# Performance work log

Measured on AMD Instinct MI355X. Metric: run time of the kernel, lower is better.

The kernel has to match this reference:

```python
import jax, jax.numpy as jnp
import numpy as np

B, N, DIM = 4, 8192, 1024
HEADS, DIM_HEAD = 16, 64


def setup_inputs() -> dict:
    key = jax.random.key(0)
    ks = jax.random.split(key, 6)
    s = 1.0 / np.sqrt(DIM_HEAD)
    so = 1.0 / np.sqrt(HEADS * DIM_HEAD)
    return {
        "x": jax.random.normal(ks[0], (B, N, DIM), dtype=jnp.float32),
        "Wq": jax.random.uniform(ks[1], (DIM_HEAD, DIM_HEAD), jnp.float32, -s, s),
        "Wk": jax.random.uniform(ks[2], (DIM_HEAD, DIM_HEAD), jnp.float32, -s, s),
        "Wv": jax.random.uniform(ks[3], (DIM_HEAD, DIM_HEAD), jnp.float32, -s, s),
        "Wo": jax.random.uniform(ks[4], (DIM, HEADS * DIM_HEAD), jnp.float32, -so, so),
        "bo": jax.random.uniform(ks[5], (DIM,), jnp.float32, -so, so),
    }


def reference(x, Wq, Wk, Wv, Wo, bo):
    Bs, Ns, Cs = x.shape
    # [B, H, N, Dh]
    xh = x.reshape(Bs, Ns, HEADS, DIM_HEAD).transpose(0, 2, 1, 3)
    # torch Linear: y = x @ W.T
    q = jnp.einsum('bhnd,ed->bhne', xh, Wq)
    k = jnp.einsum('bhnd,ed->bhne', xh, Wk)
    v = jnp.einsum('bhnd,ed->bhne', xh, Wv)
    # k^T v: [B, H, Dh, Dh], normalized by N (dropout is identity, p=0)
    dots = jnp.einsum('bhnd,bhne->bhde', k, v) / float(Ns)
    res = jnp.einsum('bhnd,bhde->bhne', q, dots)
    # b h n d -> b n (h d)
    res = res.transpose(0, 2, 1, 3).reshape(Bs, Ns, HEADS * DIM_HEAD)
    return res @ Wo.T + bo
```

## Files before the change

### kernel.cpp

```cpp
#include <hip/hip_runtime.h>

#define DIMC 1024
#define NSEQ 8192
#define DH 64

typedef __attribute__((ext_vector_type(8))) short short8;
typedef __attribute__((ext_vector_type(4))) float f32x4;

__device__ __forceinline__ short f2bf(float f) {
  union { float f; unsigned u; } v; v.f = f;
  unsigned r = v.u + 0x7FFFu + ((v.u >> 16) & 1u);
  return (short)(r >> 16);
}

__device__ __forceinline__ unsigned pack_bf2(float a, float b) {
  union { float f; unsigned u; } va, vb;
  va.f = a; vb.f = b;
  unsigned ua = va.u + 0x8000u;
  unsigned ub = vb.u + 0x8000u;
  return (ua >> 16) | (ub & 0xFFFF0000u);
}

__device__ __forceinline__ void gload_lds16(const void* g, void* l) {
  __builtin_amdgcn_global_load_lds(
      (const __attribute__((address_space(1))) void*)g,
      (__attribute__((address_space(3))) void*)l, 16, 0, 0);
}

__global__ __launch_bounds__(64) void gram_kernel(const float* __restrict__ x,
                                                  float* __restrict__ Gpart,
                                                  short* __restrict__ xbf) {
  int chunk = blockIdx.x, bh = blockIdx.y;
  int b = bh >> 4, h = bh & 15;
  int t = threadIdx.x;
  __shared__ __align__(16) float rows[16 * 64];
  const float* xb = x + ((size_t)b * NSEQ) * DIMC + h * DH;
  short* xo = xbf ? xbf + ((size_t)b * NSEQ) * DIMC + h * DH : (short*)0;
  int d0 = (t >> 3) * 8, e0 = (t & 7) * 8;
  float acc[8][8] = {};
  float4 v[4];
#pragma unroll
  for (int i = 0; i < 4; i++) {
    int f4 = i * 64 + t;
    v[i] = *(const float4*)(xb + (size_t)(chunk * 256 + (f4 >> 4)) * DIMC + (f4 & 15) * 4);
  }
  for (int it = 0; it < 16; it++) {
    __syncthreads();
#pragma unroll
    for (int i = 0; i < 4; i++) ((float4*)rows)[i * 64 + t] = v[i];
    __syncthreads();
    if (xo) {
#pragma unroll
      for (int i = 0; i < 4; i++) {
        int f4 = i * 64 + t;
        int row = chunk * 256 + it * 16 + (f4 >> 4), col = (f4 & 15) * 4;
        uint2 pw = {pack_bf2(v[i].x, v[i].y), pack_bf2(v[i].z, v[i].w)};
        *(uint2*)(xo + (size_t)row * DIMC + col) = pw;
      }
    }
    if (it < 15) {
      int nbase = chunk * 256 + (it + 1) * 16;
#pragma unroll
      for (int i = 0; i < 4; i++) {
        int f4 = i * 64 + t;
        v[i] = *(const float4*)(xb + (size_t)(nbase + (f4 >> 4)) * DIMC + (f4 & 15) * 4);
      }
    }
#pragma unroll
    for (int r = 0; r < 16; r++) {
      float xd[8], xe[8];
      *(float4*)&xd[0] = *(const float4*)&rows[r * 64 + d0];
      *(float4*)&xd[4] = *(const float4*)&rows[r * 64 + d0 + 4];
      *(float4*)&xe[0] = *(const float4*)&rows[r * 64 + e0];
      *(float4*)&xe[4] = *(const float4*)&rows[r * 64 + e0 + 4];
#pragma unroll
      for (int i = 0; i < 8; i++)
#pragma unroll
        for (int j = 0; j < 8; j++) acc[i][j] = fmaf(xd[i], xe[j], acc[i][j]);
    }
  }
  float* gp = Gpart + (size_t)chunk * (64 * 4096) + (size_t)bh * 4096;
#pragma unroll
  for (int i = 0; i < 8; i++)
#pragma unroll
    for (int j = 0; j < 8; j++) gp[(d0 + i) * 64 + e0 + j] = acc[i][j];
}

__global__ void reduce_g(const float* __restrict__ Gpart, float* __restrict__ G) {
  int i = blockIdx.x * 256 + threadIdx.x;
  float s = 0.f;
#pragma unroll
  for (int p = 0; p < 32; p++) s += Gpart[(size_t)p * (64 * 4096) + i];
  G[i] = s;
}

__global__ __launch_bounds__(256) void combine_kernel(
    const float* __restrict__ G, const float* __restrict__ Wq,
    const float* __restrict__ Wk, const float* __restrict__ Wv,
    const float* __restrict__ Wo, short* __restrict__ WbigT) {
  int bh = blockIdx.x, qt = blockIdx.y;
  int b = bh >> 4, h = bh & 15;
  int t = threadIdx.x;
  __shared__ __align__(16) float sG[4096];
  __shared__ __align__(16) float sW[4096];
  __shared__ __align__(16) float sA[4096];
  __shared__ __align__(16) float sM[4096];

  for (int i = t; i < 4096; i += 256) sG[i] = G[(size_t)bh * 4096 + i];
  for (int i = t; i < 4096; i += 256) sW[i] = Wk[i];
  __syncthreads();

  int d0 = (t >> 4) * 4, e0 = (t & 15) * 4;
  {
    float a[4][4] = {};
    for (int fg = 0; fg < 16; fg++) {
      float wk[4][4], g4[4][4];
#pragma unroll
      for (int i = 0; i < 4; i++) *(float4*)wk[i] = *(const float4*)&sW[(d0 + i) * 64 + fg * 4];
#pragma unroll
      for (int ff = 0; ff < 4; ff++) *(float4*)g4[ff] = *(const float4*)&sG[(fg * 4 + ff) * 64 + e0];
#pragma unroll
      for (int i = 0; i < 4; i++)
#pragma unroll
        for (int ff = 0; ff < 4; ff++)
#pragma unroll
          for (int j = 0; j < 4; j++) a[i][j] = fmaf(wk[i][ff], g4[ff][j], a[i][j]);
    }
#pragma unroll
    for (int i = 0; i < 4; i++)
#pragma unroll
      for (int j = 0; j < 4; j++) sA[(d0 + i) * 64 + e0 + j] = a[i][j];
  }
  __syncthreads();
  for (int i = t; i < 4096; i += 256) sW[i] = Wv[i];
  __syncthreads();
  {
    float a[4][4] = {};
    for (int fgi = 0; fgi < 16; fgi++) {
      int fg = (fgi + (t & 15)) & 15;
      float t1[4][4], wv[4][4];
#pragma unroll
      for (int i = 0; i < 4; i++) *(float4*)t1[i] = *(const float4*)&sA[(d0 + i) * 64 + fg * 4];
#pragma unroll
      for (int j = 0; j < 4; j++) *(float4*)wv[j] = *(const float4*)&sW[(e0 + j) * 64 + fg * 4];
#pragma unroll
      for (int i = 0; i < 4; i++)
#pragma unroll
        for (int j = 0; j < 4; j++)
#pragma unroll
          for (int ff = 0; ff < 4; ff++) a[i][j] = fmaf(t1[i][ff], wv[j][ff], a[i][j]);
    }
    __syncthreads();
#pragma unroll
    for (int i = 0; i < 4; i++)
#pragma unroll
      for (int j = 0; j < 4; j++) sG[(d0 + i) * 64 + e0 + j] = a[i][j];
  }
  __syncthreads();
  for (int i = t; i < 4096; i += 256) sW[i] = Wq[i];
  __syncthreads();
  {
    float a[4][4] = {};
    for (int f = 0; f < 64; f++) {
      float wq[4], t2[4];
      *(float4*)wq = *(const float4*)&sW[f * 64 + d0];
      *(float4*)t2 = *(const float4*)&sG[f * 64 + e0];
#pragma unroll
      for (int i = 0; i < 4; i++)
#pragma unroll
        for (int j = 0; j < 4; j++) a[i][j] = fmaf(wq[i], t2[j], a[i][j]);
    }
#pragma unroll
    for (int i = 0; i < 4; i++)
#pragma unroll
      for (int j = 0; j < 4; j++) sM[(d0 + i) * 64 + e0 + j] = a[i][j] * (1.0f / 8192.0f);
  }
  __syncthreads();
  int dd0 = (t & 15) * 4, cl0 = (t >> 4) * 4;
  for (int cc = qt * 2; cc < qt * 2 + 2; cc++) {
    int c0 = cc * 64;
    for (int i = t; i < 4096; i += 256)
      sW[i] = Wo[(size_t)(c0 + (i >> 6)) * DIMC + h * DH + (i & 63)];
    __syncthreads();
    float a[4][4] = {};
    for (int egi = 0; egi < 16; egi++) {
      int eg = (egi + (t & 15)) & 15;
      float m4[4][4], wo4[4][4];
#pragma unroll
      for (int i = 0; i < 4; i++) *(float4*)m4[i] = *(const float4*)&sM[(dd0 + i) * 64 + eg * 4];
#pragma unroll
      for (int j = 0; j < 4; j++) *(float4*)wo4[j] = *(const float4*)&sW[(cl0 + j) * 64 + eg * 4];
#pragma unroll
      for (int i = 0; i < 4; i++)
#pragma unroll
        for (int j = 0; j < 4; j++)
#pragma unroll
          for (int ff = 0; ff < 4; ff++) a[i][j] = fmaf(m4[i][ff], wo4[j][ff], a[i][j]);
    }
#pragma unroll
    for (int j = 0; j < 4; j++) {
      uint2 pw = {pack_bf2(a[0][j], a[1][j]), pack_bf2(a[2][j], a[3][j])};
      *(uint2*)&WbigT[((size_t)b << 20) + (size_t)(c0 + cl0 + j) * DIMC + h * DH + dd0] = pw;
    }
    __syncthreads();
  }
}

__global__ __launch_bounds__(256, 3) void gemm_small(
    const float* __restrict__ x, const short* __restrict__ WbigT,
    const float* __restrict__ bo, float* __restrict__ out) {
  int bid = blockIdx.x;
  int xcd = bid & 7, r = bid >> 3;
  int g = r >> 5, q = r & 31;
  int m_blk = g * 32 + xcd * 4 + (q >> 3);
  int n_blk = q & 7;
  int b = m_blk >> 6;
  int row0 = m_blk * 128;
  int c0 = n_blk * 128;

  __shared__ __align__(16) short As[128 * 32];
  __shared__ __align__(16) short Bs[128 * 32];

  int t = threadIdx.x;
  int lane = t & 63, wave = t >> 6;
  int wm = wave >> 1, wn = wave & 1;
  int quad = lane >> 4, ln = lane & 15;

  f32x4 acc[4][4];
#pragma unroll
  for (int i = 0; i < 4; i++)
#pragma unroll
    for (int j = 0; j < 4; j++) acc[i][j] = (f32x4){0.f, 0.f, 0.f, 0.f};

  const short* Bbase = WbigT + ((size_t)b << 20);

  int e_base[2], crow_[2], lc_[2];
#pragma unroll
  for (int L = 0; L < 2; L++) {
    int e = (wave * 2 + L) * 512 + lane * 8;
    e_base[L] = e;
    int crow = e >> 5;
    crow_[L] = crow;
    lc_[L] = ((e >> 3) & 3) ^ ((crow >> 1) & 3);
  }

  for (int kt = 0; kt < 32; kt++) {
    int k0 = kt * 32;
    __syncthreads();
#pragma unroll
    for (int L = 0; L < 2; L++)
      gload_lds16(Bbase + (size_t)(c0 + crow_[L]) * DIMC + k0 + lc_[L] * 8, &Bs[e_base[L]]);
#pragma unroll
    for (int qq = 0; qq < 2; qq++) {
      int elem = qq * 2048 + wave * 512 + lane * 8;
      int m = elem >> 5, kk = elem & 31;
      const float* gp = x + (size_t)(row0 + m) * DIMC + k0 + kk;
      float4 v0 = *(const float4*)gp;
      float4 v1 = *(const float4*)(gp + 4);
      unsigned w0 = pack_bf2(v0.x, v0.y), w1 = pack_bf2(v0.z, v0.w);
      unsigned w2 = pack_bf2(v1.x, v1.y), w3 = pack_bf2(v1.z, v1.w);
      unsigned tmp[4] = {w0, w1, w2, w3};
      int pe = ((elem >> 3) & 3) ^ ((m >> 1) & 3);
      *(short8*)&As[m * 32 + pe * 8] = *(short8*)tmp;
    }
    __syncthreads();
    short8 afrag[4], bfrag[4];
#pragma unroll
    for (int i = 0; i < 4; i++) {
      int ar = wm * 64 + i * 16 + ln;
      afrag[i] = *(const short8*)&As[ar * 32 + (quad ^ ((ar >> 1) & 3)) * 8];
      int br = wn * 64 + i * 16 + ln;
      bfrag[i] = *(const short8*)&Bs[br * 32 + (quad ^ ((br >> 1) & 3)) * 8];
    }
#pragma unroll
    for (int i = 0; i < 4; i++)
#pragma unroll
      for (int j = 0; j < 4; j++)
        acc[i][j] = __builtin_amdgcn_mfma_f32_16x16x32_bf16(afrag[i], bfrag[j], acc[i][j], 0, 0, 0);
  }

  float bov[4];
#pragma unroll
  for (int j = 0; j < 4; j++) bov[j] = bo[c0 + wn * 64 + j * 16 + ln];
#pragma unroll
  for (int i = 0; i < 4; i++)
#pragma unroll
    for (int j = 0; j < 4; j++) {
      int col = c0 + wn * 64 + j * 16 + ln;
#pragma unroll
      for (int rr = 0; rr < 4; rr++) {
        int row = row0 + wm * 64 + i * 16 + quad * 4 + rr;
        out[(size_t)row * DIMC + col] = acc[i][j][rr] + bov[j];
      }
    }
}

__global__ __launch_bounds__(256, 3) void gemm_big(
    const short* __restrict__ xbf, const short* __restrict__ WbigT,
    const float* __restrict__ bo, float* __restrict__ out) {
  int bid = blockIdx.x;
  int xcd = bid & 7, r = bid >> 3;
  int g = r >> 5, q = r & 31;
  int m_blk = g * 32 + xcd * 4 + (q >> 3);
  int n_blk = q & 7;
  int b = m_blk >> 6;
  int row0 = m_blk * 128;
  int c0 = n_blk * 128;

  __shared__ __align__(16) short As[128 * 32];
  __shared__ __align__(16) short Bs[128 * 32];

  int t = threadIdx.x;
  int lane = t & 63, wave = t >> 6;
  int wm = wave >> 1, wn = wave & 1;
  int quad = lane >> 4, ln = lane & 15;

  f32x4 acc[4][4];
#pragma unroll
  for (int i = 0; i < 4; i++)
#pragma unroll
    for (int j = 0; j < 4; j++) acc[i][j] = (f32x4){0.f, 0.f, 0.f, 0.f};

  const short* Bbase = WbigT + ((size_t)b << 20);

  int e_base[2];
  const short* Asrc[2];
  const short* Bsrc[2];
#pragma unroll
  for (int L = 0; L < 2; L++) {
    int e = (wave * 2 + L) * 512 + lane * 8;
    e_base[L] = e;
    int row = e >> 5;
    int lc = ((e >> 3) & 3) ^ ((row >> 1) & 3);
    Asrc[L] = xbf + (size_t)(row0 + row) * DIMC + lc * 8;
    Bsrc[L] = Bbase + (size_t)(c0 + row) * DIMC + lc * 8;
  }

  for (int kt = 0; kt < 32; kt++) {
    int k0 = kt * 32;
    __syncthreads();
#pragma unroll
    for (int L = 0; L < 2; L++) gload_lds16(Asrc[L] + k0, &As[e_base[L]]);
#pragma unroll
    for (int L = 0; L < 2; L++) gload_lds16(Bsrc[L] + k0, &Bs[e_base[L]]);
    __syncthreads();
    short8 afrag[4], bfrag[4];
#pragma unroll
    for (int i = 0; i < 4; i++) {
      int ar = wm * 64 + i * 16 + ln;
      afrag[i] = *(const short8*)&As[ar * 32 + (quad ^ ((ar >> 1) & 3)) * 8];
      int br = wn * 64 + i * 16 + ln;
      bfrag[i] = *(const short8*)&Bs[br * 32 + (quad ^ ((br >> 1) & 3)) * 8];
    }
#pragma unroll
    for (int i = 0; i < 4; i++)
#pragma unroll
      for (int j = 0; j < 4; j++)
        acc[i][j] = __builtin_amdgcn_mfma_f32_16x16x32_bf16(afrag[i], bfrag[j], acc[i][j], 0, 0, 0);
  }

  float bov[4];
#pragma unroll
  for (int j = 0; j < 4; j++) bov[j] = bo[c0 + wn * 64 + j * 16 + ln];
#pragma unroll
  for (int i = 0; i < 4; i++)
#pragma unroll
    for (int j = 0; j < 4; j++) {
      int col = c0 + wn * 64 + j * 16 + ln;
#pragma unroll
      for (int rr = 0; rr < 4; rr++) {
        int row = row0 + wm * 64 + i * 16 + quad * 4 + rr;
        out[(size_t)row * DIMC + col] = acc[i][j][rr] + bov[j];
      }
    }
}

extern "C" void kernel_launch(void* const* d_in, const int* in_sizes, int n_in,
                              void* d_out, int out_size, void* d_ws, size_t ws_size,
                              hipStream_t stream) {
  const float* x  = (const float*)d_in[0];
  const float* Wq = (const float*)d_in[1];
  const float* Wk = (const float*)d_in[2];
  const float* Wv = (const float*)d_in[3];
  const float* Wo = (const float*)d_in[4];
  const float* bo = (const float*)d_in[5];
  float* out = (float*)d_out;
  (void)in_sizes; (void)n_in; (void)out_size;

  if (ws_size >= ((size_t)105 << 20)) {
    short* xbf   = (short*)d_ws;
    float* Gpart = (float*)((char*)d_ws + ((size_t)64 << 20));
    float* G     = (float*)((char*)d_ws + ((size_t)96 << 20));
    short* WbigT = (short*)((char*)d_ws + ((size_t)97 << 20));
    gram_kernel<<<dim3(32, 64), 64, 0, stream>>>(x, Gpart, xbf);
    reduce_g<<<1024, 256, 0, stream>>>(Gpart, G);
    combine_kernel<<<dim3(64, 8), 256, 0, stream>>>(G, Wq, Wk, Wv, Wo, WbigT);
    gemm_big<<<2048, 256, 0, stream>>>(xbf, WbigT, bo, out);
  } else {
    float* Gpart = (float*)d_ws;
    float* G     = (float*)((char*)d_ws + ((size_t)32 << 20));
    short* WbigT = (short*)((char*)d_ws + ((size_t)33 << 20));
    gram_kernel<<<dim3(32, 64), 64, 0, stream>>>(x, Gpart, (short*)0);
    reduce_g<<<1024, 256, 0, stream>>>(Gpart, G);
    combine_kernel<<<dim3(64, 8), 256, 0, stream>>>(G, Wq, Wk, Wv, Wo, WbigT);
    gemm_small<<<2048, 256, 0, stream>>>(x, WbigT, bo, out);
  }
}
```

Before: 381.2 us.

## Rewrite big GEMM with 256x256 tiles, 512 threads and double-buffered async LDS loads

The final bf16 GEMM moves from 128x128 tiles with K=32 single-buffered steps to 256x256 tiles with K=64 steps. Loads go through global_load_lds into double-buffered LDS, and vmcnt waits let the next stage's copies overlap the MFMA work. Each wave now computes 128x64, so more MFMAs run per LDS fragment load, and s_setprio raises priority around the MFMA bursts. The grid shrinks to 512 blocks with 128KB of LDS per block, which costs occupancy, and the tail wave across the CUs may be uneven.

```diff
diff --git a/kernel.cpp b/kernel.cpp
--- a/kernel.cpp
+++ b/kernel.cpp
@@ -295,82 +295,102 @@
     }
 }
 
-__global__ __launch_bounds__(256, 3) void gemm_big(
+__global__ __launch_bounds__(512, 2) void gemm_big2(
     const short* __restrict__ xbf, const short* __restrict__ WbigT,
     const float* __restrict__ bo, float* __restrict__ out) {
   int bid = blockIdx.x;
   int xcd = bid & 7, r = bid >> 3;
-  int g = r >> 5, q = r & 31;
-  int m_blk = g * 32 + xcd * 4 + (q >> 3);
-  int n_blk = q & 7;
-  int b = m_blk >> 6;
-  int row0 = m_blk * 128;
-  int c0 = n_blk * 128;
-
-  __shared__ __align__(16) short As[128 * 32];
-  __shared__ __align__(16) short Bs[128 * 32];
+  int m_blk = xcd * 16 + (r >> 2);
+  int n_blk = r & 3;
+  int b = m_blk >> 5;
+  size_t row0 = (size_t)m_blk * 256;
+  int c0 = n_blk * 256;
+
+  __shared__ __align__(16) short As[2][256 * 64];
+  __shared__ __align__(16) short Bs[2][256 * 64];
 
   int t = threadIdx.x;
   int lane = t & 63, wave = t >> 6;
-  int wm = wave >> 1, wn = wave & 1;
+  int wm = wave >> 2, wn = wave & 3;
   int quad = lane >> 4, ln = lane & 15;
 
-  f32x4 acc[4][4];
-#pragma unroll
-  for (int i = 0; i < 4; i++)
+  f32x4 acc[8][4];
+#pragma unroll
+  for (int i = 0; i < 8; i++)
 #pragma unroll
     for (int j = 0; j < 4; j++) acc[i][j] = (f32x4){0.f, 0.f, 0.f, 0.f};
 
   const short* Bbase = WbigT + ((size_t)b << 20);
 
-  int e_base[2];
-  const short* Asrc[2];
-  const short* Bsrc[2];
-#pragma unroll
-  for (int L = 0; L < 2; L++) {
-    int e = (wave * 2 + L) * 512 + lane * 8;
-    e_base[L] = e;
-    int row = e >> 5;
-    int lc = ((e >> 3) & 3) ^ ((row >> 1) & 3);
-    Asrc[L] = xbf + (size_t)(row0 + row) * DIMC + lc * 8;
-    Bsrc[L] = Bbase + (size_t)(c0 + row) * DIMC + lc * 8;
-  }
-
-  for (int kt = 0; kt < 32; kt++) {
-    int k0 = kt * 32;
-    __syncthreads();
-#pragma unroll
-    for (int L = 0; L < 2; L++) gload_lds16(Asrc[L] + k0, &As[e_base[L]]);
-#pragma unroll
-    for (int L = 0; L < 2; L++) gload_lds16(Bsrc[L] + k0, &Bs[e_base[L]]);
-    __syncthreads();
-    short8 afrag[4], bfrag[4];
-#pragma unroll
-    for (int i = 0; i < 4; i++) {
-      int ar = wm * 64 + i * 16 + ln;
-      afrag[i] = *(const short8*)&As[ar * 32 + (quad ^ ((ar >> 1) & 3)) * 8];
-      int br = wn * 64 + i * 16 + ln;
-      bfrag[i] = *(const short8*)&Bs[br * 32 + (quad ^ ((br >> 1) & 3)) * 8];
-    }
-#pragma unroll
-    for (int i = 0; i < 4; i++)
-#pragma unroll
-      for (int j = 0; j < 4; j++)
-        acc[i][j] = __builtin_amdgcn_mfma_f32_16x16x32_bf16(afrag[i], bfrag[j], acc[i][j], 0, 0, 0);
+  const short* Asrc[4];
+  const short* Bsrc[4];
+  int doff[4];
+#pragma unroll
+  for (int s = 0; s < 4; s++) {
+    int p = s * 512 + t;
+    int row = p >> 3;
+    int cl = (p & 7) ^ (row & 7);
+    doff[s] = p * 8;
+    Asrc[s] = xbf + (row0 + row) * (size_t)DIMC + cl * 8;
+    Bsrc[s] = Bbase + (size_t)(c0 + row) * DIMC + cl * 8;
+  }
+
+  auto stage = [&](int kt, int u) {
+    int k0 = kt * 64;
+#pragma unroll
+    for (int s = 0; s < 4; s++) gload_lds16(Asrc[s] + k0, &As[u][doff[s]]);
+#pragma unroll
+    for (int s = 0; s < 4; s++) gload_lds16(Bsrc[s] + k0, &Bs[u][doff[s]]);
+  };
+
+  stage(0, 0);
+  stage(1, 1);
+
+  for (int kt = 0; kt < 16; kt++) {
+    if (kt < 15) asm volatile("s_waitcnt vmcnt(8)" ::: "memory");
+    else         asm volatile("s_waitcnt vmcnt(0)" ::: "memory");
+    __builtin_amdgcn_s_barrier();
+    const short* Ab = As[kt & 1];
+    const short* Bb = Bs[kt & 1];
+#pragma unroll
+    for (int kk = 0; kk < 2; kk++) {
+      short8 af[8];
+      short8 bf4[4];
+#pragma unroll
+      for (int i = 0; i < 8; i++) {
+        int ar = wm * 128 + i * 16 + ln;
+        af[i] = *(const short8*)&Ab[ar * 64 + (((kk * 4 + quad) ^ (ar & 7)) << 3)];
+      }
+#pragma unroll
+      for (int j = 0; j < 4; j++) {
+        int br = wn * 64 + j * 16 + ln;
+        bf4[j] = *(const short8*)&Bb[br * 64 + (((kk * 4 + quad) ^ (br & 7)) << 3)];
+      }
+      __builtin_amdgcn_s_setprio(1);
+#pragma unroll
+      for (int i = 0; i < 8; i++)
+#pragma unroll
+        for (int j = 0; j < 4; j++)
+          acc[i][j] = __builtin_amdgcn_mfma_f32_16x16x32_bf16(af[i], bf4[j], acc[i][j], 0, 0, 0);
+      __builtin_amdgcn_s_setprio(0);
+    }
+    __builtin_amdgcn_s_barrier();
+    asm volatile("" ::: "memory");
+    if (kt < 14) stage(kt + 2, kt & 1);
   }
 
   float bov[4];
 #pragma unroll
   for (int j = 0; j < 4; j++) bov[j] = bo[c0 + wn * 64 + j * 16 + ln];
 #pragma unroll
-  for (int i = 0; i < 4; i++)
+  for (int i = 0; i < 8; i++)
 #pragma unroll
     for (int j = 0; j < 4; j++) {
       int col = c0 + wn * 64 + j * 16 + ln;
 #pragma unroll
       for (int rr = 0; rr < 4; rr++) {
-        int row = row0 + wm * 64 + i * 16 + quad * 4 + rr;
-        out[(size_t)row * DIMC + col] = acc[i][j][rr] + bov[j];
+        size_t row = row0 + wm * 128 + i * 16 + quad * 4 + rr;
+        out[row * DIMC + col] = acc[i][j][rr] + bov[j];
       }
     }
 }
@@ -395,7 +415,7 @@
     gram_kernel<<<dim3(32, 64), 64, 0, stream>>>(x, Gpart, xbf);
     reduce_g<<<1024, 256, 0, stream>>>(Gpart, G);
     combine_kernel<<<dim3(64, 8), 256, 0, stream>>>(G, Wq, Wk, Wv, Wo, WbigT);
-    gemm_big<<<2048, 256, 0, stream>>>(xbf, WbigT, bo, out);
+    gemm_big2<<<512, 512, 0, stream>>>(xbf, WbigT, bo, out);
   } else {
     float* Gpart = (float*)d_ws;
     float* G     = (float*)((char*)d_ws + ((size_t)32 << 20));
```

Measured after the change: 384.9 us. Within noise of the previous version (+1.0%).

## Compute per-head Gram matrix with split-bf16 MFMA instead of scalar FMA

Applied to the files above, without the earlier changes.

Adds a new Gram kernel that splits each fp32 x value into high and low bf16 parts and accumulates X^T X with three bf16 MFMA products (hi*hi, hi*lo, lo*hi). Each 256-thread block covers 1024 rows with four wavefronts, stages transposed tiles in a swizzled LDS layout, and prefetches the next rows into registers. It still writes the bf16 copy of x for the later GEMM and keeps the same Gpart layout of 32 partials per head. The aim is to move the Gram computation off scalar FP32 ALUs and onto matrix cores, at the cost of a small precision loss from the dropped lo*lo term.

```diff
diff --git a/kernel.cpp b/kernel.cpp
--- a/kernel.cpp
+++ b/kernel.cpp
@@ -21,10 +21,129 @@
   return (ua >> 16) | (ub & 0xFFFF0000u);
 }
 
+__device__ __forceinline__ unsigned bfbits(float f) {
+  union { float f; unsigned u; } v; v.f = f;
+  return (v.u + 0x8000u) >> 16;
+}
+__device__ __forceinline__ float bf2f(unsigned hb) {
+  union { unsigned u; float f; } v; v.u = hb << 16;
+  return v.f;
+}
+
 __device__ __forceinline__ void gload_lds16(const void* g, void* l) {
   __builtin_amdgcn_global_load_lds(
       (const __attribute__((address_space(1))) void*)g,
       (__attribute__((address_space(3))) void*)l, 16, 0, 0);
+}
+
+__global__ __launch_bounds__(256) void gram2_kernel(const float* __restrict__ x,
+                                                    float* __restrict__ Gpart,
+                                                    short* __restrict__ xbf) {
+  int chunk = blockIdx.x, bh = blockIdx.y;
+  int b = bh >> 4, h = bh & 15;
+  int t = threadIdx.x;
+  int w = t >> 6, l = t & 63;
+  int quad = l >> 4, ln = l & 15;
+
+  __shared__ __align__(16) short XT[4][2][64 * 32];
+  short* XH = &XT[w][0][0];
+  short* XL = &XT[w][1][0];
+
+  size_t rowbase = (size_t)b * NSEQ + (size_t)chunk * 1024 + w * 256;
+  const float* xb = x + rowbase * DIMC + h * DH;
+  short* xo = xbf + rowbase * DIMC + h * DH;
+
+  f32x4 acc[4][4];
+#pragma unroll
+  for (int i = 0; i < 4; i++)
+#pragma unroll
+    for (int j = 0; j < 4; j++) acc[i][j] = (f32x4){0.f, 0.f, 0.f, 0.f};
+
+  int woff[4][4];
+#pragma unroll
+  for (int q = 0; q < 4; q++) {
+    int kk = 8 * q + 2 * quad;
+    int kp = kk ^ ((ln & 3) << 3);
+#pragma unroll
+    for (int i = 0; i < 4; i++) {
+      int d = ln * 4 + i;
+      woff[q][i] = d * 32 + kp;
+    }
+  }
+  int roff[4];
+  {
+    int k0 = (quad * 8) ^ ((ln >> 2) << 3);
+#pragma unroll
+    for (int i = 0; i < 4; i++) roff[i] = (i * 16 + ln) * 32 + k0;
+  }
+
+  float4 cur[4][2];
+#pragma unroll
+  for (int q = 0; q < 4; q++)
+#pragma unroll
+    for (int r = 0; r < 2; r++)
+      cur[q][r] = *(const float4*)(xb + (size_t)(8 * q + 2 * quad + r) * DIMC + ln * 4);
+
+  for (int ks = 0; ks < 8; ks++) {
+    float4 nxt[4][2];
+    if (ks < 7) {
+      int nb = (ks + 1) * 32;
+#pragma unroll
+      for (int q = 0; q < 4; q++)
+#pragma unroll
+        for (int r = 0; r < 2; r++)
+          nxt[q][r] = *(const float4*)(xb + (size_t)(nb + 8 * q + 2 * quad + r) * DIMC + ln * 4);
+    }
+#pragma unroll
+    for (int q = 0; q < 4; q++) {
+      unsigned h0[4], h1[4], l0[4], l1[4];
+#pragma unroll
+      for (int i = 0; i < 4; i++) {
+        float a = cur[q][0][i], bb = cur[q][1][i];
+        h0[i] = bfbits(a); l0[i] = bfbits(a - bf2f(h0[i]));
+        h1[i] = bfbits(bb); l1[i] = bfbits(bb - bf2f(h1[i]));
+      }
+      int grow = ks * 32 + 8 * q + 2 * quad;
+      uint2 p0 = {h0[0] | (h0[1] << 16), h0[2] | (h0[3] << 16)};
+      uint2 p1 = {h1[0] | (h1[1] << 16), h1[2] | (h1[3] << 16)};
+      *(uint2*)(xo + (size_t)grow * DIMC + ln * 4) = p0;
+      *(uint2*)(xo + (size_t)(grow + 1) * DIMC + ln * 4) = p1;
+#pragma unroll
+      for (int i = 0; i < 4; i++) {
+        *(unsigned*)&XH[woff[q][i]] = h0[i] | (h1[i] << 16);
+        *(unsigned*)&XL[woff[q][i]] = l0[i] | (l1[i] << 16);
+      }
+    }
+    short8 hf[4], lf[4];
+#pragma unroll
+    for (int i = 0; i < 4; i++) {
+      hf[i] = *(const short8*)&XH[roff[i]];
+      lf[i] = *(const short8*)&XL[roff[i]];
+    }
+#pragma unroll
+    for (int i = 0; i < 4; i++)
+#pragma unroll
+      for (int j = 0; j < 4; j++) {
+        acc[i][j] = __builtin_amdgcn_mfma_f32_16x16x32_bf16(hf[i], hf[j], acc[i][j], 0, 0, 0);
+        acc[i][j] = __builtin_amdgcn_mfma_f32_16x16x32_bf16(hf[i], lf[j], acc[i][j], 0, 0, 0);
+        acc[i][j] = __builtin_amdgcn_mfma_f32_16x16x32_bf16(lf[i], hf[j], acc[i][j], 0, 0, 0);
+      }
+#pragma unroll
+    for (int q = 0; q < 4; q++)
+#pragma unroll
+      for (int r = 0; r < 2; r++) cur[q][r] = nxt[q][r];
+  }
+
+  float* gp = Gpart + (size_t)(chunk * 4 + w) * (64 * 4096) + (size_t)bh * 4096;
+#pragma unroll
+  for (int i = 0; i < 4; i++)
+#pragma unroll
+    for (int j = 0; j < 4; j++)
+#pragma unroll
+      for (int r = 0; r < 4; r++) {
+        int d = i * 16 + quad * 4 + r, e = j * 16 + ln;
+        gp[d * 64 + e] = acc[i][j][r];
+      }
 }
 
 __global__ __launch_bounds__(64) void gram_kernel(const float* __restrict__ x,
@@ -392,7 +511,7 @@
     float* Gpart = (float*)((char*)d_ws + ((size_t)64 << 20));
     float* G     = (float*)((char*)d_ws + ((size_t)96 << 20));
     short* WbigT = (short*)((char*)d_ws + ((size_t)97 << 20));
-    gram_kernel<<<dim3(32, 64), 64, 0, stream>>>(x, Gpart, xbf);
+    gram2_kernel<<<dim3(8, 64), 256, 0, stream>>>(x, Gpart, xbf);
     reduce_g<<<1024, 256, 0, stream>>>(Gpart, G);
     combine_kernel<<<dim3(64, 8), 256, 0, stream>>>(G, Wq, Wk, Wv, Wo, WbigT);
     gemm_big<<<2048, 256, 0, stream>>>(xbf, WbigT, bo, out);
```

Result: no change. 375.4 us (-1.5%).
